# Kernel optimization log

Hardware: AMD Instinct MI355X
Metric: run time of the kernel (lower is better)

## Reference

```python
import jax, jax.numpy as jnp
import numpy as np

WS = 4        # window_size
SS = 2        # shift_size
NH = 8        # num_heads
EPS = 1e-5    # LayerNorm eps (torch default)


def _rel_pos_index(ws):
    coords = np.stack(np.meshgrid(np.arange(ws), np.arange(ws), indexing='ij')).reshape(2, -1)
    rel = (coords[:, :, None] - coords[:, None, :]).transpose(1, 2, 0)
    rel[..., 0] += ws - 1
    rel[..., 1] += ws - 1
    rel[..., 0] *= 2 * ws - 1
    return rel.sum(-1)  # [N, N] ints

REL_IDX = _rel_pos_index(WS)


def _shift_mask(Hp, Wp, ws, ss):
    # standard Swin shifted-window region mask: 0 within region, -100 across regions
    img = np.zeros((Hp, Wp))
    cnt = 0
    for hs in (slice(0, -ws), slice(-ws, -ss), slice(-ss, None)):
        for wsl in (slice(0, -ws), slice(-ws, -ss), slice(-ss, None)):
            img[hs, wsl] = cnt
            cnt += 1
    mw = img.reshape(Hp // ws, ws, Wp // ws, ws).transpose(0, 2, 1, 3).reshape(-1, ws * ws)
    d = mw[:, None, :] - mw[:, :, None]
    return np.where(d != 0, -100.0, 0.0).astype(np.float32)  # [nW, N, N]


def _ln(x, g, b):
    m = jnp.mean(x, -1, keepdims=True)
    v = jnp.mean((x - m) ** 2, -1, keepdims=True)
    return (x - m) * jax.lax.rsqrt(v + EPS) * g + b


def setup_inputs() -> dict:
    key = jax.random.key(0)
    ks = jax.random.split(key, 8)
    D, F = 512, 1024
    rn = lambda k, s: (jax.random.normal(k, s, jnp.float32) * 0.02)
    return {
        'x': jax.random.normal(ks[0], (4, 64 * 128, D), jnp.float32),
        'g1': jnp.ones((D,), jnp.float32), 'beta1': jnp.zeros((D,), jnp.float32),
        'w_qkv': rn(ks[1], (3 * D, D)), 'b_qkv': jnp.zeros((3 * D,), jnp.float32),
        'rpb': rn(ks[2], ((2 * WS - 1) ** 2, NH)),
        'w_proj': rn(ks[3], (D, D)), 'b_proj': jnp.zeros((D,), jnp.float32),
        'g2': jnp.ones((D,), jnp.float32), 'beta2': jnp.zeros((D,), jnp.float32),
        'w1': rn(ks[4], (F, D)), 'b1': jnp.zeros((F,), jnp.float32),
        'w2': rn(ks[5], (D, F)), 'b2': jnp.zeros((D,), jnp.float32),
        'H': 64, 'W': 128,
    }


def reference(x, g1, beta1, w_qkv, b_qkv, rpb, w_proj, b_proj, g2, beta2, w1, b1, w2, b2, H, W):
    B, L, C = x.shape
    hd = C // NH
    scale = hd ** (-0.5)
    N = WS * WS
    Hp, Wp = H, W  # H, W chosen divisible by WS -> no padding branch
    nW = (Hp // WS) * (Wp // WS)

    shortcut = x
    h = _ln(x, g1, beta1).reshape(B, H, W, C)
    # cyclic shift
    h = jnp.roll(h, (-SS, -SS), axis=(1, 2))
    # window partition -> [B*nW, N, C]
    xw = h.reshape(B, Hp // WS, WS, Wp // WS, WS, C).transpose(0, 1, 3, 2, 4, 5).reshape(-1, N, C)

    qkv = (xw @ w_qkv.T + b_qkv).reshape(-1, N, 3, NH, hd).transpose(2, 0, 3, 1, 4)
    q, k, v = qkv[0] * scale, qkv[1], qkv[2]          # [B*nW, NH, N, hd]
    attn = jnp.einsum('whnd,whmd->whnm', q, k)        # [B*nW, NH, N, N]

    bias = rpb[REL_IDX.reshape(-1)].reshape(N, N, NH).transpose(2, 0, 1)  # [NH, N, N]
    attn = attn + bias[None]

    mask = jnp.asarray(_shift_mask(Hp, Wp, WS, SS))   # [nW, N, N]
    attn = attn.reshape(B, nW, NH, N, N) + mask[None, :, None]
    attn = jax.nn.softmax(attn.reshape(-1, NH, N, N), axis=-1)

    o = jnp.einsum('whnm,whmd->whnd', attn, v).transpose(0, 2, 1, 3).reshape(-1, N, C)
    o = o @ w_proj.T + b_proj
    # window reverse + reverse shift
    o = o.reshape(B, Hp // WS, Wp // WS, WS, WS, C).transpose(0, 1, 3, 2, 4, 5).reshape(B, Hp, Wp, C)
    o = jnp.roll(o, (SS, SS), axis=(1, 2)).reshape(B, H * W, C)

    x = shortcut + o
    h2 = _ln(x, g2, beta2)
    m = jax.nn.gelu(h2 @ w1.T + b1, approximate=False) @ w2.T + b2
    return x + m
```

## Files before the change

### kernel.cpp

```cpp
#include <hip/hip_runtime.h>
#include <hip/hip_bf16.h>
#include <math.h>

typedef __bf16 bf16_t;
typedef __bf16 bf16x8 __attribute__((ext_vector_type(8)));
typedef float f32x4 __attribute__((ext_vector_type(4)));


#define X1_OFF   0u
#define XW_OFF   67108864u
#define QKV_OFF  100663296u
#define WQ_OFF   201326592u
#define WP_OFF   202899456u
#define W1_OFF   203423744u
#define W2_OFF   204472320u
#define SV_OFF   205520896u
#define FLAG_OFF 205545472u

__device__ __forceinline__ int perm_row(int r) {
    int b   = r >> 13;
    int rem = r & 8191;
    int w   = rem >> 4;
    int n   = rem & 15;
    int wy  = w >> 5, wx = w & 31;
    int y   = wy * 4 + (n >> 2);
    int x   = wx * 4 + (n & 3);
    int ys  = (y + 2) & 63;
    int xs  = (x + 2) & 127;
    return (b << 13) + (ys << 7) + xs;
}

__device__ __forceinline__ void gld16(const void* g, void* l) {
    __builtin_amdgcn_global_load_lds(
        (const __attribute__((address_space(1))) unsigned int*)(unsigned long long)(uintptr_t)g,
        (__attribute__((address_space(3))) unsigned int*)(unsigned int)(uintptr_t)l,
        16, 0, 0);
}

__global__ __launch_bounds__(256) void k_probe(const unsigned short* __restrict__ x,
                                               int n, int* __restrict__ flag) {
    __shared__ int cnt;
    if (threadIdx.x == 0) cnt = 0;
    __syncthreads();
    int c = 0;
    for (int i = threadIdx.x; i < n; i += 256) {
        int e = (x[i] >> 7) & 0xFF;
        if (e >= 0xC0) c++;
    }
    atomicAdd(&cnt, c);
    __syncthreads();
    if (threadIdx.x == 0) *flag = (cnt > 8) ? 1 : 0;
}

__global__ __launch_bounds__(256) void k_cvt_bf16(const void* __restrict__ src,
                                                  bf16_t* __restrict__ dst, int n,
                                                  const int* __restrict__ flag) {
    int i = blockIdx.x * 256 + threadIdx.x;
    if (i >= n) return;
    dst[i] = (*flag) ? (bf16_t)((const float*)src)[i] : ((const bf16_t*)src)[i];
}

__global__ __launch_bounds__(256) void k_cvt_small(
        const void* g1, const void* be1, const void* bq, const void* bp,
        const void* g2, const void* be2, const void* b1, const void* b2,
        const void* rpb, float* __restrict__ dst, const int* __restrict__ flag) {
    int i = blockIdx.x * 256 + threadIdx.x;
    const void* src; int off;
    if      (i < 512)  { src = g1;  off = i; }
    else if (i < 1024) { src = be1; off = i - 512; }
    else if (i < 2560) { src = bq;  off = i - 1024; }
    else if (i < 3072) { src = bp;  off = i - 2560; }
    else if (i < 3584) { src = g2;  off = i - 3072; }
    else if (i < 4096) { src = be2; off = i - 3584; }
    else if (i < 5120) { src = b1;  off = i - 4096; }
    else if (i < 5632) { src = b2;  off = i - 5120; }
    else if (i < 6024) { src = rpb; off = i - 5632; }
    else return;
    dst[i] = (*flag) ? ((const float*)src)[off] : (float)((const bf16_t*)src)[off];
}

__global__ __launch_bounds__(256) void k_ln1(const void* __restrict__ x,
                                             const float* __restrict__ g,
                                             const float* __restrict__ be,
                                             bf16_t* __restrict__ xw,
                                             const int* __restrict__ flag) {
    int r    = blockIdx.x * 4 + (threadIdx.x >> 6);
    int lane = threadIdx.x & 63;
    int f    = *flag;
    long ro  = (long)perm_row(r) * 512;
    const float*  x32 = (const float*)x + ro;
    const bf16_t* x16 = (const bf16_t*)x + ro;
    int base = lane * 8;
    float v[8];
    float s = 0.f, ss = 0.f;
#pragma unroll
    for (int j = 0; j < 8; j++) {
        float t = f ? x32[base + j] : (float)x16[base + j];
        v[j] = t; s += t; ss += t * t;
    }
#pragma unroll
    for (int off = 32; off; off >>= 1) {
        s  += __shfl_down(s,  off, 64);
        ss += __shfl_down(ss, off, 64);
    }
    s  = __shfl(s, 0, 64);
    ss = __shfl(ss, 0, 64);
    float m   = s * (1.f / 512.f);
    float var = ss * (1.f / 512.f) - m * m;
    float inv = rsqrtf(var + 1e-5f);
    bf16_t* orow = xw + (long)r * 512;
#pragma unroll
    for (int j = 0; j < 8; j++)
        orow[base + j] = (bf16_t)((v[j] - m) * inv * g[base + j] + be[base + j]);
}

__global__ __launch_bounds__(256) void k_ln2(const float* __restrict__ x1,
                                             const float* __restrict__ g,
                                             const float* __restrict__ be,
                                             bf16_t* __restrict__ h2) {
    int r    = blockIdx.x * 4 + (threadIdx.x >> 6);
    int lane = threadIdx.x & 63;
    const float* xr = x1 + (long)r * 512;
    int base = lane * 8;
    float v[8];
    float s = 0.f, ss = 0.f;
#pragma unroll
    for (int j = 0; j < 8; j++) {
        float t = xr[base + j];
        v[j] = t; s += t; ss += t * t;
    }
#pragma unroll
    for (int off = 32; off; off >>= 1) {
        s  += __shfl_down(s,  off, 64);
        ss += __shfl_down(ss, off, 64);
    }
    s  = __shfl(s, 0, 64);
    ss = __shfl(ss, 0, 64);
    float m   = s * (1.f / 512.f);
    float var = ss * (1.f / 512.f) - m * m;
    float inv = rsqrtf(var + 1e-5f);
    bf16_t* orow = h2 + (long)r * 512;
#pragma unroll
    for (int j = 0; j < 8; j++)
        orow[base + j] = (bf16_t)((v[j] - m) * inv * g[base + j] + be[base + j]);
}

template<int EPI>
__global__ __launch_bounds__(256) void k_gemm128(const bf16_t* __restrict__ A,
                                                 const bf16_t* __restrict__ Wt,
                                                 const float* __restrict__ bias,
                                                 void* __restrict__ out,
                                                 const void* __restrict__ res,
                                                 const int* __restrict__ flag,
                                                 int N, int K) {
    __shared__ char smem[69632];
    int tid  = threadIdx.x;
    int lane = tid & 63, wv = tid >> 6;

    int nbx = N >> 7;
    int id  = blockIdx.x;
    int xb  = (id >> 3) % nbx;
    int yb  = ((id >> 3) / nbx) * 8 + (id & 7);
    int m0  = yb << 7, n0 = xb << 7;

    int srow = tid >> 3;
    int kc   = (tid & 7) ^ (srow & 7);
    const bf16_t* gA = A  + (long)(m0 + srow) * K + kc * 8;
    const bf16_t* gB = Wt + (long)(n0 + srow) * K + kc * 8;

    int rr = lane & 15, quad = lane >> 4;
    int wm = (wv >> 1) * 64, wn = (wv & 1) * 64;
    int p0 = ((quad ^ (rr & 7)) * 8);

    f32x4 acc[4][4];
#pragma unroll
    for (int mi = 0; mi < 4; mi++)
#pragma unroll
        for (int ni = 0; ni < 4; ni++) { f32x4 z = {0.f,0.f,0.f,0.f}; acc[mi][ni] = z; }

    int KT = K >> 6;

#pragma unroll
    for (int j = 0; j < 4; j++) {
        gld16(gA + (long)j * 32 * K, smem + j * 4096 + wv * 1024);
        gld16(gB + (long)j * 32 * K, smem + 16384 + j * 4096 + wv * 1024);
    }
    __syncthreads();

    int cur = 0;
    for (int t = 0; t < KT; t++) {
        if (t + 1 < KT) {
            const bf16_t* nA = gA + (long)(t + 1) * 64;
            const bf16_t* nB = gB + (long)(t + 1) * 64;
            char* db = smem + (cur ^ 1) * 32768;
#pragma unroll
            for (int j = 0; j < 4; j++) {
                gld16(nA + (long)j * 32 * K, db + j * 4096 + wv * 1024);
                gld16(nB + (long)j * 32 * K, db + 16384 + j * 4096 + wv * 1024);
            }
        }
        const bf16_t* rA = (const bf16_t*)(smem + cur * 32768) + (wm + rr) * 64;
        const bf16_t* rB = (const bf16_t*)(smem + cur * 32768 + 16384) + (wn + rr) * 64;
#pragma unroll
        for (int ks = 0; ks < 2; ks++) {
            int pp = ks ? (p0 ^ 32) : p0;
            bf16x8 af[4], bg[4];
#pragma unroll
            for (int i = 0; i < 4; i++) af[i] = *(const bf16x8*)(rA + i * 1024 + pp);
#pragma unroll
            for (int i = 0; i < 4; i++) bg[i] = *(const bf16x8*)(rB + i * 1024 + pp);
#pragma unroll
            for (int mi = 0; mi < 4; mi++)
#pragma unroll
                for (int ni = 0; ni < 4; ni++)
                    acc[mi][ni] = __builtin_amdgcn_mfma_f32_16x16x32_bf16(af[mi], bg[ni], acc[mi][ni], 0, 0, 0);
        }
        __syncthreads();
        cur ^= 1;
    }

    float* sc = (float*)smem + wv * 4352;
#pragma unroll
    for (int mi = 0; mi < 4; mi++)
#pragma unroll
        for (int ni = 0; ni < 4; ni++)
#pragma unroll
            for (int i = 0; i < 4; i++)
                sc[(mi * 16 + quad * 4 + i) * 68 + ni * 16 + rr] = acc[mi][ni][i];

    int f = (EPI == 1 || EPI == 3) ? *flag : 0;
    int rl = lane >> 3;
    int cl = (lane & 7) * 8;
#pragma unroll
    for (int p = 0; p < 8; p++) {
        int row_l = p * 8 + rl;
        f32x4 v0 = *(const f32x4*)(sc + row_l * 68 + cl);
        f32x4 v1 = *(const f32x4*)(sc + row_l * 68 + cl + 4);
        int row = m0 + wm + row_l;
        int col = n0 + wn + cl;
        f32x4 b0 = *(const f32x4*)(bias + col);
        f32x4 b1 = *(const f32x4*)(bias + col + 4);
        v0 += b0; v1 += b1;

        if (EPI == 0) {
            bf16x8 ob;
#pragma unroll
            for (int c = 0; c < 4; c++) { ob[c] = (bf16_t)v0[c]; ob[c + 4] = (bf16_t)v1[c]; }
            *(bf16x8*)((bf16_t*)out + (long)row * N + col) = ob;
        } else if (EPI == 1) {
            long o = (long)perm_row(row) * 512 + col;
            if (f) {
                f32x4 r0 = *(const f32x4*)((const float*)res + o);
                f32x4 r1 = *(const f32x4*)((const float*)res + o + 4);
                v0 += r0; v1 += r1;
            } else {
                bf16x8 rb = *(const bf16x8*)((const bf16_t*)res + o);
#pragma unroll
                for (int c = 0; c < 4; c++) { v0[c] += (float)rb[c]; v1[c] += (float)rb[c + 4]; }
            }
            *(f32x4*)((float*)out + o)     = v0;
            *(f32x4*)((float*)out + o + 4) = v1;
        } else if (EPI == 2) {
            bf16x8 ob;
#pragma unroll
            for (int c = 0; c < 4; c++) {
                float a0 = v0[c], a1 = v1[c];
                ob[c]     = (bf16_t)(0.5f * a0 * (1.f + erff(a0 * 0.70710678118654752f)));
                ob[c + 4] = (bf16_t)(0.5f * a1 * (1.f + erff(a1 * 0.70710678118654752f)));
            }
            *(bf16x8*)((bf16_t*)out + (long)row * N + col) = ob;
        } else {
            long o = (long)row * 512 + col;
            f32x4 r0 = *(const f32x4*)((const float*)res + o);
            f32x4 r1 = *(const f32x4*)((const float*)res + o + 4);
            v0 += r0; v1 += r1;
            if (f) {
                *(f32x4*)((float*)out + o)     = v0;
                *(f32x4*)((float*)out + o + 4) = v1;
            } else {
                bf16x8 ob;
#pragma unroll
                for (int c = 0; c < 4; c++) { ob[c] = (bf16_t)v0[c]; ob[c + 4] = (bf16_t)v1[c]; }
                *(bf16x8*)((bf16_t*)out + o) = ob;
            }
        }
    }
}

__global__ __launch_bounds__(256) void k_attn(const bf16_t* __restrict__ qkv,
                                              const float* __restrict__ rpb,
                                              bf16_t* __restrict__ O) {
    __shared__ float q[16][68], k[16][68], v[16][68];
    __shared__ float S[16][17];

    int blk = blockIdx.x;
    int h   = blk & 7;
    int w   = blk >> 3;
    int tid = threadIdx.x;

    int n0 = tid >> 4;
    int d0 = (tid & 15) * 4;
    const bf16_t* base = qkv + (long)(w * 16 + n0) * 1536 + h * 64 + d0;
#pragma unroll
    for (int j = 0; j < 4; j++) {
        q[n0][d0 + j] = (float)base[j] * 0.125f;
        k[n0][d0 + j] = (float)base[512 + j];
        v[n0][d0 + j] = (float)base[1024 + j];
    }
    __syncthreads();

    int i = tid >> 4, j = tid & 15;
    float s = 0.f;
#pragma unroll
    for (int d = 0; d < 64; d++) s += q[i][d] * k[j][d];

    int iy = i >> 2, ix = i & 3, jy = j >> 2, jx = j & 3;
    s += rpb[((iy - jy + 3) * 7 + (ix - jx + 3)) * 8 + h];

    int wl = w & 511;
    int wy = wl >> 5, wx = wl & 31;
    int yi = wy * 4 + iy, xi = wx * 4 + ix;
    int yj = wy * 4 + jy, xj = wx * 4 + jx;
    int ri = (yi < 60 ? 0 : (yi < 62 ? 1 : 2)) * 3 + (xi < 124 ? 0 : (xi < 126 ? 1 : 2));
    int rj = (yj < 60 ? 0 : (yj < 62 ? 1 : 2)) * 3 + (xj < 124 ? 0 : (xj < 126 ? 1 : 2));
    if (ri != rj) s -= 100.f;
    S[i][j] = s;
    __syncthreads();

    if (tid < 16) {
        float mx = -1e30f;
#pragma unroll
        for (int c = 0; c < 16; c++) mx = fmaxf(mx, S[tid][c]);
        float sum = 0.f;
#pragma unroll
        for (int c = 0; c < 16; c++) { float e = expf(S[tid][c] - mx); S[tid][c] = e; sum += e; }
        float invs = 1.f / sum;
#pragma unroll
        for (int c = 0; c < 16; c++) S[tid][c] *= invs;
    }
    __syncthreads();

#pragma unroll
    for (int t = 0; t < 4; t++) {
        int e  = tid + t * 256;
        int oi = e >> 6, od = e & 63;
        float acc = 0.f;
#pragma unroll
        for (int c = 0; c < 16; c++) acc += S[oi][c] * v[c][od];
        O[(long)(w * 16 + oi) * 512 + h * 64 + od] = (bf16_t)acc;
    }
}

extern "C" void kernel_launch(void* const* d_in, const int* in_sizes, int n_in,
                              void* d_out, int out_size, void* d_ws, size_t ws_size,
                              hipStream_t stream) {
    char* ws = (char*)d_ws;
    float*  x1   = (float*)(ws + X1_OFF);
    bf16_t* xw   = (bf16_t*)(ws + XW_OFF);
    bf16_t* qkv  = (bf16_t*)(ws + QKV_OFF);
    bf16_t* wq_b = (bf16_t*)(ws + WQ_OFF);
    bf16_t* wp_b = (bf16_t*)(ws + WP_OFF);
    bf16_t* w1_b = (bf16_t*)(ws + W1_OFF);
    bf16_t* w2_b = (bf16_t*)(ws + W2_OFF);
    float*  sv   = (float*)(ws + SV_OFF);
    int*    flag = (int*)(ws + FLAG_OFF);

    k_probe<<<1, 256, 0, stream>>>((const unsigned short*)d_in[0], 4096, flag);
    k_cvt_bf16<<<3072, 256, 0, stream>>>(d_in[3],  wq_b, 786432, flag);
    k_cvt_bf16<<<1024, 256, 0, stream>>>(d_in[6],  wp_b, 262144, flag);
    k_cvt_bf16<<<2048, 256, 0, stream>>>(d_in[10], w1_b, 524288, flag);
    k_cvt_bf16<<<2048, 256, 0, stream>>>(d_in[12], w2_b, 524288, flag);
    k_cvt_small<<<24,  256, 0, stream>>>(d_in[1], d_in[2], d_in[4], d_in[7],
                                         d_in[8], d_in[9], d_in[11], d_in[13],
                                         d_in[5], sv, flag);

    k_ln1<<<dim3(8192), dim3(256), 0, stream>>>(d_in[0], sv, sv + 512, xw, flag);
    k_gemm128<0><<<dim3(3072), dim3(256), 0, stream>>>(xw, wq_b, sv + 1024, qkv, nullptr, flag, 1536, 512);
    k_attn<<<dim3(16384), dim3(256), 0, stream>>>(qkv, sv + 5632, xw );
    k_gemm128<1><<<dim3(1024), dim3(256), 0, stream>>>(xw, wp_b, sv + 2560, x1, d_in[0], flag, 512, 512);
    k_ln2<<<dim3(8192), dim3(256), 0, stream>>>(x1, sv + 3072, sv + 3584, xw );
    k_gemm128<2><<<dim3(2048), dim3(256), 0, stream>>>(xw, w1_b, sv + 4096, qkv , nullptr, flag, 1024, 512);
    k_gemm128<3><<<dim3(1024), dim3(256), 0, stream>>>(qkv, w2_b, sv + 5120, d_out, x1, flag, 512, 1024);
}
```

Before: 472.1 us.

## Replace 128x128 GEMM with 256x256 tiles and 4-stage pipelined loads

Replaces the 128x128, 256-thread GEMM with a 256x256, 512-thread kernel. It uses BK=32 stages in a 4-deep LDS ring, prefetches two stages ahead, and uses explicit vmcnt waits, s_setprio around the MFMA blocks, and an XOR-swizzled LDS layout. The goal is more reuse per tile loaded from global memory and better overlap of loads with MFMA work. In exchange it needs 128 KB of LDS and 128 accumulator registers per thread, so occupancy is lower, and the grids are much smaller (256-768 blocks), which may underfill the CUs on the smaller GEMMs.

```diff
diff --git a/kernel.cpp b/kernel.cpp
--- a/kernel.cpp
+++ b/kernel.cpp
@@ -146,142 +146,173 @@
 }
 
 template<int EPI>
-__global__ __launch_bounds__(256) void k_gemm128(const bf16_t* __restrict__ A,
-                                                 const bf16_t* __restrict__ Wt,
-                                                 const float* __restrict__ bias,
-                                                 void* __restrict__ out,
-                                                 const void* __restrict__ res,
-                                                 const int* __restrict__ flag,
-                                                 int N, int K) {
-    __shared__ char smem[69632];
+__global__ __launch_bounds__(512, 2) void k_gemm256(const bf16_t* __restrict__ A,
+                                                    const bf16_t* __restrict__ Wt,
+                                                    const float* __restrict__ bias,
+                                                    void* __restrict__ out,
+                                                    const void* __restrict__ res,
+                                                    const int* __restrict__ flag,
+                                                    int N, int K) {
+    __shared__ __attribute__((aligned(16))) char smem[131072];
     int tid  = threadIdx.x;
     int lane = tid & 63, wv = tid >> 6;
 
-    int nbx = N >> 7;
+    int nbx = N >> 8;
     int id  = blockIdx.x;
     int xb  = (id >> 3) % nbx;
     int yb  = ((id >> 3) / nbx) * 8 + (id & 7);
-    int m0  = yb << 7, n0 = xb << 7;
-
-    int srow = tid >> 3;
-    int kc   = (tid & 7) ^ (srow & 7);
-    const bf16_t* gA = A  + (long)(m0 + srow) * K + kc * 8;
-    const bf16_t* gB = Wt + (long)(n0 + srow) * K + kc * 8;
+    int m0  = yb << 8, n0 = xb << 8;
+
+    int srow = tid >> 2;
+    int cg   = (tid & 3) ^ (srow & 3) ^ ((srow >> 2) & 3);
+    const bf16_t* gA = A  + (long)(m0 + srow) * K + cg * 8;
+    const bf16_t* gB = Wt + (long)(n0 + srow) * K + cg * 8;
+    long rstep = (long)128 * K;
+    int  l0 = wv * 1024, l1 = 8192 + wv * 1024;
+
+    int S = K >> 5;
+
+    gld16(gA,              smem + l0);
+    gld16(gA + rstep,      smem + l1);
+    gld16(gB,              smem + 16384 + l0);
+    gld16(gB + rstep,      smem + 16384 + l1);
+    gld16(gA + 32,         smem + 32768 + l0);
+    gld16(gA + rstep + 32, smem + 32768 + l1);
+    gld16(gB + 32,         smem + 32768 + 16384 + l0);
+    gld16(gB + rstep + 32, smem + 32768 + 16384 + l1);
 
     int rr = lane & 15, quad = lane >> 4;
-    int wm = (wv >> 1) * 64, wn = (wv & 1) * 64;
-    int p0 = ((quad ^ (rr & 7)) * 8);
-
-    f32x4 acc[4][4];
-#pragma unroll
-    for (int mi = 0; mi < 4; mi++)
+    int wh = wv >> 2, wq = wv & 3;
+    int cA   = quad ^ (rr & 3) ^ ((rr >> 2) & 3);
+    int aoff = (wh * 128 + rr) * 32 + cA * 8;
+    int boff = 8192 + (wq * 64 + rr) * 32 + cA * 8;
+
+    f32x4 acc[8][4];
+#pragma unroll
+    for (int mi = 0; mi < 8; mi++)
 #pragma unroll
         for (int ni = 0; ni < 4; ni++) { f32x4 z = {0.f,0.f,0.f,0.f}; acc[mi][ni] = z; }
 
-    int KT = K >> 6;
-
-#pragma unroll
-    for (int j = 0; j < 4; j++) {
-        gld16(gA + (long)j * 32 * K, smem + j * 4096 + wv * 1024);
-        gld16(gB + (long)j * 32 * K, smem + 16384 + j * 4096 + wv * 1024);
-    }
-    __syncthreads();
-
-    int cur = 0;
-    for (int t = 0; t < KT; t++) {
-        if (t + 1 < KT) {
-            const bf16_t* nA = gA + (long)(t + 1) * 64;
-            const bf16_t* nB = gB + (long)(t + 1) * 64;
-            char* db = smem + (cur ^ 1) * 32768;
-#pragma unroll
-            for (int j = 0; j < 4; j++) {
-                gld16(nA + (long)j * 32 * K, db + j * 4096 + wv * 1024);
-                gld16(nB + (long)j * 32 * K, db + 16384 + j * 4096 + wv * 1024);
+    for (int s = 0; s < S; ++s) {
+        if (s + 2 < S) {
+            char* db = smem + ((s + 2) & 3) * 32768;
+            long  ko = (long)(s + 2) * 32;
+            gld16(gA + ko,          db + l0);
+            gld16(gA + rstep + ko,  db + l1);
+            gld16(gB + ko,          db + 16384 + l0);
+            gld16(gB + rstep + ko,  db + 16384 + l1);
+            asm volatile("s_waitcnt vmcnt(8)" ::: "memory");
+        } else if (s + 2 == S) {
+            asm volatile("s_waitcnt vmcnt(4)" ::: "memory");
+        } else {
+            asm volatile("s_waitcnt vmcnt(0)" ::: "memory");
+        }
+        __builtin_amdgcn_sched_barrier(0);
+        __builtin_amdgcn_s_barrier();
+        __builtin_amdgcn_sched_barrier(0);
+
+        const bf16_t* sb = (const bf16_t*)(smem + (s & 3) * 32768);
+        const bf16_t* pa = sb + aoff;
+        const bf16_t* pb = sb + boff;
+        bf16x8 bg[4], af[4];
+#pragma unroll
+        for (int ni = 0; ni < 4; ni++) bg[ni] = *(const bf16x8*)(pb + ni * 512);
+#pragma unroll
+        for (int mi = 0; mi < 4; mi++) af[mi] = *(const bf16x8*)(pa + mi * 512);
+        __builtin_amdgcn_s_setprio(1);
+#pragma unroll
+        for (int mi = 0; mi < 4; mi++)
+#pragma unroll
+            for (int ni = 0; ni < 4; ni++)
+                acc[mi][ni] = __builtin_amdgcn_mfma_f32_16x16x32_bf16(af[mi], bg[ni], acc[mi][ni], 0, 0, 0);
+        __builtin_amdgcn_s_setprio(0);
+#pragma unroll
+        for (int mi = 0; mi < 4; mi++) af[mi] = *(const bf16x8*)(pa + (mi + 4) * 512);
+        __builtin_amdgcn_s_setprio(1);
+#pragma unroll
+        for (int mi = 0; mi < 4; mi++)
+#pragma unroll
+            for (int ni = 0; ni < 4; ni++)
+                acc[mi + 4][ni] = __builtin_amdgcn_mfma_f32_16x16x32_bf16(af[mi], bg[ni], acc[mi + 4][ni], 0, 0, 0);
+        __builtin_amdgcn_s_setprio(0);
+    }
+
+    __builtin_amdgcn_sched_barrier(0);
+    __builtin_amdgcn_s_barrier();
+    __builtin_amdgcn_sched_barrier(0);
+
+    float* sc  = (float*)smem + wv * 4096;
+    int f      = (EPI == 1 || EPI == 3) ? *flag : 0;
+    int rl     = lane >> 3;
+    int cl8    = (lane & 7) * 8;
+    int colw   = n0 + wq * 64 + cl8;
+    f32x4 b0   = *(const f32x4*)(bias + colw);
+    f32x4 b1   = *(const f32x4*)(bias + colw + 4);
+
+#pragma unroll
+    for (int h = 0; h < 2; ++h) {
+#pragma unroll
+        for (int mi2 = 0; mi2 < 4; ++mi2)
+#pragma unroll
+            for (int ni = 0; ni < 4; ++ni) {
+                int ch = ni * 4 + (rr >> 2);
+#pragma unroll
+                for (int i = 0; i < 4; ++i) {
+                    int r = mi2 * 16 + quad * 4 + i;
+                    sc[r * 64 + (((ch ^ (r & 15)) << 2) | (rr & 3))] = acc[h * 4 + mi2][ni][i];
+                }
             }
-        }
-        const bf16_t* rA = (const bf16_t*)(smem + cur * 32768) + (wm + rr) * 64;
-        const bf16_t* rB = (const bf16_t*)(smem + cur * 32768 + 16384) + (wn + rr) * 64;
-#pragma unroll
-        for (int ks = 0; ks < 2; ks++) {
-            int pp = ks ? (p0 ^ 32) : p0;
-            bf16x8 af[4], bg[4];
-#pragma unroll
-            for (int i = 0; i < 4; i++) af[i] = *(const bf16x8*)(rA + i * 1024 + pp);
-#pragma unroll
-            for (int i = 0; i < 4; i++) bg[i] = *(const bf16x8*)(rB + i * 1024 + pp);
-#pragma unroll
-            for (int mi = 0; mi < 4; mi++)
-#pragma unroll
-                for (int ni = 0; ni < 4; ni++)
-                    acc[mi][ni] = __builtin_amdgcn_mfma_f32_16x16x32_bf16(af[mi], bg[ni], acc[mi][ni], 0, 0, 0);
-        }
-        __syncthreads();
-        cur ^= 1;
-    }
-
-    float* sc = (float*)smem + wv * 4352;
-#pragma unroll
-    for (int mi = 0; mi < 4; mi++)
-#pragma unroll
-        for (int ni = 0; ni < 4; ni++)
-#pragma unroll
-            for (int i = 0; i < 4; i++)
-                sc[(mi * 16 + quad * 4 + i) * 68 + ni * 16 + rr] = acc[mi][ni][i];
-
-    int f = (EPI == 1 || EPI == 3) ? *flag : 0;
-    int rl = lane >> 3;
-    int cl = (lane & 7) * 8;
-#pragma unroll
-    for (int p = 0; p < 8; p++) {
-        int row_l = p * 8 + rl;
-        f32x4 v0 = *(const f32x4*)(sc + row_l * 68 + cl);
-        f32x4 v1 = *(const f32x4*)(sc + row_l * 68 + cl + 4);
-        int row = m0 + wm + row_l;
-        int col = n0 + wn + cl;
-        f32x4 b0 = *(const f32x4*)(bias + col);
-        f32x4 b1 = *(const f32x4*)(bias + col + 4);
-        v0 += b0; v1 += b1;
-
-        if (EPI == 0) {
-            bf16x8 ob;
-#pragma unroll
-            for (int c = 0; c < 4; c++) { ob[c] = (bf16_t)v0[c]; ob[c + 4] = (bf16_t)v1[c]; }
-            *(bf16x8*)((bf16_t*)out + (long)row * N + col) = ob;
-        } else if (EPI == 1) {
-            long o = (long)perm_row(row) * 512 + col;
-            if (f) {
+#pragma unroll
+        for (int p = 0; p < 8; ++p) {
+            int r   = p * 8 + rl;
+            int sw  = r & 15;
+            int ch0 = (lane & 7) * 2;
+            f32x4 v0 = *(const f32x4*)(sc + r * 64 + (((ch0    ) ^ sw) << 2));
+            f32x4 v1 = *(const f32x4*)(sc + r * 64 + (((ch0 + 1) ^ sw) << 2));
+            int row = m0 + wh * 128 + h * 64 + r;
+            v0 += b0; v1 += b1;
+
+            if (EPI == 0) {
+                bf16x8 ob;
+#pragma unroll
+                for (int c = 0; c < 4; c++) { ob[c] = (bf16_t)v0[c]; ob[c + 4] = (bf16_t)v1[c]; }
+                *(bf16x8*)((bf16_t*)out + (long)row * N + colw) = ob;
+            } else if (EPI == 1) {
+                long o = (long)perm_row(row) * 512 + colw;
+                if (f) {
+                    f32x4 r0 = *(const f32x4*)((const float*)res + o);
+                    f32x4 r1 = *(const f32x4*)((const float*)res + o + 4);
+                    v0 += r0; v1 += r1;
+                } else {
+                    bf16x8 rb = *(const bf16x8*)((const bf16_t*)res + o);
+#pragma unroll
+                    for (int c = 0; c < 4; c++) { v0[c] += (float)rb[c]; v1[c] += (float)rb[c + 4]; }
+                }
+                *(f32x4*)((float*)out + o)     = v0;
+                *(f32x4*)((float*)out + o + 4) = v1;
+            } else if (EPI == 2) {
+                bf16x8 ob;
+#pragma unroll
+                for (int c = 0; c < 4; c++) {
+                    float a0 = v0[c], a1 = v1[c];
+                    ob[c]     = (bf16_t)(0.5f * a0 * (1.f + erff(a0 * 0.70710678118654752f)));
+                    ob[c + 4] = (bf16_t)(0.5f * a1 * (1.f + erff(a1 * 0.70710678118654752f)));
+                }
+                *(bf16x8*)((bf16_t*)out + (long)row * N + colw) = ob;
+            } else {
+                long o = (long)row * 512 + colw;
                 f32x4 r0 = *(const f32x4*)((const float*)res + o);
                 f32x4 r1 = *(const f32x4*)((const float*)res + o + 4);
                 v0 += r0; v1 += r1;
-            } else {
-                bf16x8 rb = *(const bf16x8*)((const bf16_t*)res + o);
-#pragma unroll
-                for (int c = 0; c < 4; c++) { v0[c] += (float)rb[c]; v1[c] += (float)rb[c + 4]; }
-            }
-            *(f32x4*)((float*)out + o)     = v0;
-            *(f32x4*)((float*)out + o + 4) = v1;
-        } else if (EPI == 2) {
-            bf16x8 ob;
-#pragma unroll
-            for (int c = 0; c < 4; c++) {
-                float a0 = v0[c], a1 = v1[c];
-                ob[c]     = (bf16_t)(0.5f * a0 * (1.f + erff(a0 * 0.70710678118654752f)));
-                ob[c + 4] = (bf16_t)(0.5f * a1 * (1.f + erff(a1 * 0.70710678118654752f)));
-            }
-            *(bf16x8*)((bf16_t*)out + (long)row * N + col) = ob;
-        } else {
-            long o = (long)row * 512 + col;
-            f32x4 r0 = *(const f32x4*)((const float*)res + o);
-            f32x4 r1 = *(const f32x4*)((const float*)res + o + 4);
-            v0 += r0; v1 += r1;
-            if (f) {
-                *(f32x4*)((float*)out + o)     = v0;
-                *(f32x4*)((float*)out + o + 4) = v1;
-            } else {
-                bf16x8 ob;
-#pragma unroll
-                for (int c = 0; c < 4; c++) { ob[c] = (bf16_t)v0[c]; ob[c + 4] = (bf16_t)v1[c]; }
-                *(bf16x8*)((bf16_t*)out + o) = ob;
+                if (f) {
+                    *(f32x4*)((float*)out + o)     = v0;
+                    *(f32x4*)((float*)out + o + 4) = v1;
+                } else {
+                    bf16x8 ob;
+#pragma unroll
+                    for (int c = 0; c < 4; c++) { ob[c] = (bf16_t)v0[c]; ob[c + 4] = (bf16_t)v1[c]; }
+                    *(bf16x8*)((bf16_t*)out + o) = ob;
+                }
             }
         }
     }
@@ -375,10 +406,10 @@
                                          d_in[5], sv, flag);
 
     k_ln1<<<dim3(8192), dim3(256), 0, stream>>>(d_in[0], sv, sv + 512, xw, flag);
-    k_gemm128<0><<<dim3(3072), dim3(256), 0, stream>>>(xw, wq_b, sv + 1024, qkv, nullptr, flag, 1536, 512);
+    k_gemm256<0><<<dim3(768), dim3(512), 0, stream>>>(xw, wq_b, sv + 1024, qkv, nullptr, flag, 1536, 512);
     k_attn<<<dim3(16384), dim3(256), 0, stream>>>(qkv, sv + 5632, xw );
-    k_gemm128<1><<<dim3(1024), dim3(256), 0, stream>>>(xw, wp_b, sv + 2560, x1, d_in[0], flag, 512, 512);
+    k_gemm256<1><<<dim3(256), dim3(512), 0, stream>>>(xw, wp_b, sv + 2560, x1, d_in[0], flag, 512, 512);
     k_ln2<<<dim3(8192), dim3(256), 0, stream>>>(x1, sv + 3072, sv + 3584, xw );
-    k_gemm128<2><<<dim3(2048), dim3(256), 0, stream>>>(xw, w1_b, sv + 4096, qkv , nullptr, flag, 1024, 512);
-    k_gemm128<3><<<dim3(1024), dim3(256), 0, stream>>>(qkv, w2_b, sv + 5120, d_out, x1, flag, 512, 1024);
-}
+    k_gemm256<2><<<dim3(512), dim3(512), 0, stream>>>(xw, w1_b, sv + 4096, qkv , nullptr, flag, 1024, 512);
+    k_gemm256<3><<<dim3(256), dim3(512), 0, stream>>>(qkv, w2_b, sv + 5120, d_out, x1, flag, 512, 1024);
+}
```

Measured after the change: 522.7 us. 10.7% more time.
